# Kernel tuning notes

Measured on AMD Instinct MI355X. Metric: run time of the kernel, lower is better.

## Reference

```python
import jax, jax.numpy as jnp
import numpy as np

B, CIR_LEN, AUX_DIM, T, CD, DS, DCONV = 16, 16384, 14, 512, 256, 16, 4
SEG = CIR_LEN // T          # 32
DI = 2 * CD                 # d_inner = 512


def layer_norm(x, g, b, eps=1e-5):
    m = jnp.mean(x, -1, keepdims=True)
    v = jnp.var(x, -1, keepdims=True)
    return (x - m) * jax.lax.rsqrt(v + eps) * g + b


def gelu(x):
    return jax.nn.gelu(x, approximate=False)  # torch default exact GELU


def selective_ssm(x, in_proj_w, conv_w, conv_b, x_proj_w, dt_proj_w, dt_proj_b, A_log, D, out_proj_w):
    # x: (B, L, CD)
    Bsz, L, _ = x.shape
    xz = x @ in_proj_w.T                      # (B, L, 2*DI)
    x_in, z = jnp.split(xz, 2, axis=-1)       # each (B, L, DI)
    # depthwise causal conv (pad d_conv-1 left, truncate to L == torch pad both + [:L])
    xp = jnp.pad(x_in, ((0, 0), (DCONV - 1, 0), (0, 0)))
    x_conv = sum(xp[:, k:k + L, :] * conv_w[:, k] for k in range(DCONV)) + conv_b
    x_conv = jax.nn.silu(x_conv)              # (B, L, DI)
    ssm_in = x_conv @ x_proj_w.T              # (B, L, 1+2*DS)
    dt_raw = ssm_in[..., :1]
    B_ssm = ssm_in[..., 1:1 + DS]             # (B, L, DS)
    C_ssm = ssm_in[..., 1 + DS:]              # (B, L, DS)
    delta = jax.nn.softplus(dt_raw @ dt_proj_w.T + dt_proj_b)      # (B, L, DI)
    A = -jnp.exp(A_log)                                            # (DI, DS)
    deltaA = jnp.exp(delta[..., None] * A)                         # (B, L, DI, DS)
    deltaB_u = delta[..., None] * B_ssm[:, :, None, :] * x_conv[..., None]

    def step(h, inp):
        dA, dBu, c = inp
        h = dA * h + dBu                       # (B, DI, DS)
        y = jnp.einsum('bds,bs->bd', h, c)     # (B, DI)
        return h, y

    h0 = jnp.zeros((Bsz, DI, DS), x.dtype)
    _, ys = jax.lax.scan(step, h0, (jnp.moveaxis(deltaA, 1, 0),
                                    jnp.moveaxis(deltaB_u, 1, 0),
                                    jnp.moveaxis(C_ssm, 1, 0)))
    y = jnp.moveaxis(ys, 0, 1)                 # (B, L, DI)
    y = y + x_conv * D
    y = y * jax.nn.silu(z)
    return y @ out_proj_w.T                    # (B, L, CD)


def setup_inputs() -> dict:
    key = jax.random.key(0)
    ks = iter(jax.random.split(key, 32))
    rn = lambda shape, s=0.02: jax.random.normal(next(ks), shape, jnp.float32) * s
    return {
        'cir': jax.random.normal(next(ks), (B, CIR_LEN), jnp.float32),
        'aux': jax.random.normal(next(ks), (B, AUX_DIM), jnp.float32),
        'cir_proj_w': rn((CD, SEG)),
        'cir_norm_g': jnp.ones((CD,)), 'cir_norm_b': jnp.zeros((CD,)),
        'aux_proj_w': rn((CD, AUX_DIM)),
        'aux_norm_g': jnp.ones((CD,)), 'aux_norm_b': jnp.zeros((CD,)),
        'm_norm_g': jnp.ones((CD,)), 'm_norm_b': jnp.zeros((CD,)),
        'in_proj_w': rn((2 * DI, CD)),
        'conv_w': rn((DI, DCONV)), 'conv_b': jnp.zeros((DI,)),
        'x_proj_w': rn((1 + 2 * DS, DI)),
        'dt_proj_w': rn((DI, 1)), 'dt_proj_b': jnp.zeros((DI,)),
        'A_log': jnp.log(jnp.broadcast_to(jnp.arange(1, DS + 1, dtype=jnp.float32), (DI, DS))),
        'D': jnp.ones((DI,)),
        'out_proj_w': rn((CD, DI)),
        'mid_w': rn((CD, CD)), 'mid_b': jnp.zeros((CD,)),
        'mid_norm_g': jnp.ones((CD,)), 'mid_norm_b': jnp.zeros((CD,)),
        'bn_g': jnp.ones((CD,)), 'bn_b': jnp.zeros((CD,)),
        'fc1_w': rn((CD // 2, CD)), 'fc1_b': jnp.zeros((CD // 2,)),
        'fc2_w': rn((1, CD // 2)), 'fc2_b': jnp.zeros((1,)),
    }


def reference(cir, aux, cir_proj_w, cir_norm_g, cir_norm_b, aux_proj_w, aux_norm_g, aux_norm_b,
              m_norm_g, m_norm_b, in_proj_w, conv_w, conv_b, x_proj_w, dt_proj_w, dt_proj_b,
              A_log, D, out_proj_w, mid_w, mid_b, mid_norm_g, mid_norm_b, bn_g, bn_b,
              fc1_w, fc1_b, fc2_w, fc2_b):
    # eval mode: dropout = identity, BatchNorm uses running stats (mean 0, var 1)
    x_seg = cir.reshape(cir.shape[0], T, SEG)
    h_cir = gelu(layer_norm(x_seg @ cir_proj_w.T, cir_norm_g, cir_norm_b))
    h_aux = gelu(layer_norm(aux @ aux_proj_w.T, aux_norm_g, aux_norm_b))[:, None, :]
    h = h_cir + h_aux                          # (B, T, CD)
    h = h + selective_ssm(layer_norm(h, m_norm_g, m_norm_b), in_proj_w, conv_w, conv_b,
                          x_proj_w, dt_proj_w, dt_proj_b, A_log, D, out_proj_w)
    hp = jnp.mean(h, axis=1)                   # AdaptiveAvgPool1d(1)
    h2 = gelu(layer_norm(hp @ mid_w.T + mid_b, mid_norm_g, mid_norm_b))
    hbn = h2 * jax.lax.rsqrt(jnp.float32(1.0 + 1e-5)) * bn_g + bn_b
    h3 = gelu(hbn @ fc1_w.T + fc1_b)
    return (h3 @ fc2_w.T + fc2_b)[:, 0]
```

## Files before the change

kernel.cpp:

```cpp
#include <hip/hip_runtime.h>
#include <hip/hip_bf16.h>

typedef __hip_bfloat16 bf16;
typedef __attribute__((ext_vector_type(8))) short short8;
typedef __attribute__((ext_vector_type(4))) float f32x4;

#define Bsz   16
#define Tn    512
#define SEG   32
#define CD    256
#define DI    512
#define DS    16
#define DCONV 4
#define BT    (Bsz*Tn)
#define NPART 32

__device__ __forceinline__ float erf_fast(float x) {
  float ax = fabsf(x);
  float t = 1.0f / (1.0f + 0.3275911f * ax);
  float p = t * (0.254829592f + t * (-0.284496736f + t * (1.421413741f +
            t * (-1.453152027f + t * 1.061405429f))));
  float r = 1.0f - p * __expf(-ax * ax);
  return copysignf(r, x);
}
__device__ __forceinline__ float gelu_f(float x) {
  return 0.5f * x * (1.0f + erf_fast(x * 0.7071067811865476f));
}
__device__ __forceinline__ float silu_f(float x) {
  return x / (1.0f + __expf(-x));
}
__device__ __forceinline__ float softplus_f(float x) {
  return fmaxf(x, 0.0f) + __logf(1.0f + __expf(-fabsf(x)));
}
__device__ __forceinline__ float bfu(unsigned short u) {
  return __uint_as_float(((unsigned int)u) << 16);
}
__device__ __forceinline__ unsigned short f2bfu(float x) {
  bf16 h = __float2bfloat16(x);
  return *(unsigned short*)&h;
}
__device__ __forceinline__ float block_sum256(float v, float* red) {
  int tid = threadIdx.x;
  #pragma unroll
  for (int off = 32; off > 0; off >>= 1) v += __shfl_down(v, off, 64);
  __syncthreads();
  if ((tid & 63) == 0) red[tid >> 6] = v;
  __syncthreads();
  return red[0] + red[1] + red[2] + red[3];
}

__global__ __launch_bounds__(256) void prep_kernel(
    const float* __restrict__ aux, const float* __restrict__ apw,
    const float* __restrict__ g, const float* __restrict__ bb,
    const float* __restrict__ in_w, const float* __restrict__ xpw,
    const float* __restrict__ cpw,
    bf16* __restrict__ w_in, bf16* __restrict__ wpad, bf16* __restrict__ cpwT,
    float* __restrict__ haux)
{
  __shared__ float red[4];
  int i = blockIdx.x * 256 + threadIdx.x;
  if (i < 262144) {
    int e = i & 7, lane = (i >> 3) & 63, k0 = (i >> 9) & 7, nb = i >> 12;
    int fr = lane & 15, q = lane >> 4;
    w_in[i] = __float2bfloat16(in_w[(size_t)(nb * 16 + fr) * 256 + k0 * 32 + q * 8 + e]);
  } else if (i < 294912) {
    int o = i - 262144;
    int e = o & 7, lane = (o >> 3) & 63, k0 = (o >> 9) & 15, nb = o >> 13;
    int fr = lane & 15, q = lane >> 4;
    int row = nb * 16 + fr, k = k0 * 32 + q * 8 + e;
    float v = 0.f;
    if (row < 32)       v = xpw[(1 + row) * 512 + k];
    else if (row == 32) v = xpw[k];
    wpad[o] = __float2bfloat16(v);
  } else {
    int o = i - 294912;
    int k = o >> 8, j = o & 255;
    cpwT[o] = __float2bfloat16(cpw[j * 32 + k]);
  }
  if (blockIdx.x < 16) {
    int b = blockIdx.x, j = threadIdx.x;
    float acc = 0.f;
    #pragma unroll
    for (int k = 0; k < 14; ++k)
      acc += aux[b * 14 + k] * apw[j * 14 + k];
    float s1 = block_sum256(acc, red);
    float s2 = block_sum256(acc * acc, red);
    float mean = s1 * (1.f / 256.f);
    float var  = s2 * (1.f / 256.f) - mean * mean;
    float xn = (acc - mean) * rsqrtf(var + 1e-5f) * g[j] + bb[j];
    haux[b * 256 + j] = gelu_f(xn);
  }
}

__global__ __launch_bounds__(512) void row_inproj_kernel(
    const float* __restrict__ cir, const bf16* __restrict__ cpwT,
    const float* __restrict__ cg, const float* __restrict__ cb,
    const float* __restrict__ mg, const float* __restrict__ mb,
    const float* __restrict__ haux, const bf16* __restrict__ w_in,
    bf16* __restrict__ xzbf, float* __restrict__ hp_part)
{
  __shared__ float hps[8][256];
  __shared__ __align__(16) unsigned short xns[16][264];
  int tid = threadIdx.x;
  int wave = tid >> 6, lane = tid & 63;
  int r0 = blockIdx.x * 16 + wave * 2;
  int b = blockIdx.x >> 5;
  int j0 = lane * 4;

  float vj[2][4] = {};
  for (int c = 0; c < 8; ++c) {
    float xk[2][4];
    #pragma unroll
    for (int r4 = 0; r4 < 2; ++r4) {
      float4 xv = ((const float4*)(cir + (size_t)(r0 + r4) * SEG))[c];
      xk[r4][0] = xv.x; xk[r4][1] = xv.y; xk[r4][2] = xv.z; xk[r4][3] = xv.w;
    }
    #pragma unroll
    for (int kk = 0; kk < 4; ++kk) {
      int k = c * 4 + kk;
      uint2 wv = *(const uint2*)((const unsigned short*)cpwT + k * 256 + j0);
      float w0 = __uint_as_float(wv.x << 16);
      float w1 = __uint_as_float(wv.x & 0xffff0000u);
      float w2 = __uint_as_float(wv.y << 16);
      float w3 = __uint_as_float(wv.y & 0xffff0000u);
      #pragma unroll
      for (int r4 = 0; r4 < 2; ++r4) {
        float xv = xk[r4][kk];
        vj[r4][0] += xv * w0; vj[r4][1] += xv * w1;
        vj[r4][2] += xv * w2; vj[r4][3] += xv * w3;
      }
    }
  }
  float s[2], q2[2];
  #pragma unroll
  for (int r4 = 0; r4 < 2; ++r4) {
    s[r4]  = vj[r4][0] + vj[r4][1] + vj[r4][2] + vj[r4][3];
    q2[r4] = vj[r4][0]*vj[r4][0] + vj[r4][1]*vj[r4][1]
           + vj[r4][2]*vj[r4][2] + vj[r4][3]*vj[r4][3];
  }
  #pragma unroll
  for (int off = 32; off > 0; off >>= 1) {
    #pragma unroll
    for (int r4 = 0; r4 < 2; ++r4) {
      s[r4]  += __shfl_xor(s[r4],  off, 64);
      q2[r4] += __shfl_xor(q2[r4], off, 64);
    }
  }
  float4 cgv = *(const float4*)(cg + j0);
  float4 cbv = *(const float4*)(cb + j0);
  float4 hxv = *(const float4*)(haux + b * 256 + j0);
  float hv[2][4];
  float hs[2], hq[2];
  #pragma unroll
  for (int r4 = 0; r4 < 2; ++r4) {
    float mean = s[r4] * (1.f/256.f);
    float var  = q2[r4] * (1.f/256.f) - mean * mean;
    float inv  = rsqrtf(var + 1e-5f);
    float g0 = gelu_f((vj[r4][0] - mean) * inv * cgv.x + cbv.x) + hxv.x;
    float g1 = gelu_f((vj[r4][1] - mean) * inv * cgv.y + cbv.y) + hxv.y;
    float g2 = gelu_f((vj[r4][2] - mean) * inv * cgv.z + cbv.z) + hxv.z;
    float g3 = gelu_f((vj[r4][3] - mean) * inv * cgv.w + cbv.w) + hxv.w;
    hv[r4][0] = g0; hv[r4][1] = g1; hv[r4][2] = g2; hv[r4][3] = g3;
    hs[r4] = g0 + g1 + g2 + g3;
    hq[r4] = g0*g0 + g1*g1 + g2*g2 + g3*g3;
  }
  #pragma unroll
  for (int off = 32; off > 0; off >>= 1) {
    #pragma unroll
    for (int r4 = 0; r4 < 2; ++r4) {
      hs[r4] += __shfl_xor(hs[r4], off, 64);
      hq[r4] += __shfl_xor(hq[r4], off, 64);
    }
  }
  float4 mgv = *(const float4*)(mg + j0);
  float4 mbv = *(const float4*)(mb + j0);
  #pragma unroll
  for (int r4 = 0; r4 < 2; ++r4) {
    float m2  = hs[r4] * (1.f/256.f);
    float v2  = hq[r4] * (1.f/256.f) - m2 * m2;
    float inv2 = rsqrtf(v2 + 1e-5f);
    unsigned int lo = (unsigned int)f2bfu((hv[r4][0] - m2) * inv2 * mgv.x + mbv.x) |
                      ((unsigned int)f2bfu((hv[r4][1] - m2) * inv2 * mgv.y + mbv.y) << 16);
    unsigned int hi = (unsigned int)f2bfu((hv[r4][2] - m2) * inv2 * mgv.z + mbv.z) |
                      ((unsigned int)f2bfu((hv[r4][3] - m2) * inv2 * mgv.w + mbv.w) << 16);
    uint2 pk; pk.x = lo; pk.y = hi;
    *(uint2*)&xns[wave * 2 + r4][j0] = pk;
  }
  #pragma unroll
  for (int q = 0; q < 4; ++q)
    hps[wave][j0 + q] = hv[0][q] + hv[1][q];
  __syncthreads();
  if (tid < 256) {
    int j = tid;
    float part = hps[0][j] + hps[1][j] + hps[2][j] + hps[3][j]
               + hps[4][j] + hps[5][j] + hps[6][j] + hps[7][j];
    hp_part[(size_t)(blockIdx.x & (NPART - 1)) * 4096 + b * 256 + j] =
        part * (1.f / 512.f);
  }
  {
    int fr = lane & 15, quad = lane >> 4;
    int rbase = blockIdx.x * 16;
    const short* Wp = (const short*)w_in;
    unsigned short* xzp = (unsigned short*)xzbf;
    #pragma unroll
    for (int nt = 0; nt < 8; ++nt) {
      int nb = wave * 8 + nt;
      f32x4 acc = {0.f, 0.f, 0.f, 0.f};
      #pragma unroll
      for (int k0 = 0; k0 < 8; ++k0) {
        int ka = k0 * 32 + quad * 8;
        short8 a = *(const short8*)&xns[fr][ka];
        short8 bb8 = *(const short8*)(Wp + (((size_t)nb * 8 + k0) * 64 + lane) * 8);
        acc = __builtin_amdgcn_mfma_f32_16x16x32_bf16(a, bb8, acc, 0, 0, 0);
      }
      int n0 = nb * 16;
      int crow = quad * 4;
      #pragma unroll
      for (int i = 0; i < 4; ++i)
        xzp[(size_t)(rbase + crow + i) * 1024 + n0 + fr] = f2bfu(acc[i]);
    }
  }
}

__global__ __launch_bounds__(512) void conv_xproj_kernel(
    const bf16* __restrict__ xzbf, const bf16* __restrict__ wpad,
    const float* __restrict__ cw, const float* __restrict__ cbv,
    float* __restrict__ ssm)
{
  __shared__ __align__(16) unsigned short xst[35][512];
  __shared__ __align__(16) unsigned short xcs[32][520];
  int c = blockIdx.x, b = blockIdx.y;
  int t0 = c * 32;
  int tid = threadIdx.x;
  const unsigned short* xzp = (const unsigned short*)xzbf;

  for (int it = tid; it < 2240; it += 512) {
    int row = it >> 6, c8 = it & 63;
    int t = t0 - 3 + row;
    uint4 v = make_uint4(0u, 0u, 0u, 0u);
    if (t >= 0)
      v = *(const uint4*)(xzp + ((size_t)((b << 9) + t)) * 1024 + c8 * 8);
    *(uint4*)&xst[row][c8 * 8] = v;
  }
  __syncthreads();

  {
    int d = tid;
    float4 w = *(const float4*)(cw + d * 4);
    float cbd = cbv[d];
    float pa = bfu(xst[0][d]), pb = bfu(xst[1][d]), pc = bfu(xst[2][d]);
    #pragma unroll
    for (int i = 0; i < 32; ++i) {
      float x = bfu(xst[3 + i][d]);
      float a = cbd + w.x * pa + w.y * pb + w.z * pc + w.w * x;
      pa = pb; pb = pc; pc = x;
      xcs[i][d] = f2bfu(silu_f(a));
    }
  }
  __syncthreads();

  {
    int wave = tid >> 6, lane = tid & 63;
    int fr = lane & 15, quad = lane >> 4;
    int mh = wave >> 2;
    int nb = wave & 3;
    int n0 = nb * 16;
    f32x4 acc = {0.f, 0.f, 0.f, 0.f};
    const short* Wp = (const short*)wpad;
    #pragma unroll
    for (int k0 = 0; k0 < 16; ++k0) {
      int ka = k0 * 32 + quad * 8;
      short8 a = *(const short8*)&xcs[mh * 16 + fr][ka];
      short8 b8 = *(const short8*)(Wp + (((size_t)nb * 16 + k0) * 64 + lane) * 8);
      acc = __builtin_amdgcn_mfma_f32_16x16x32_bf16(a, b8, acc, 0, 0, 0);
    }
    int ccol = lane & 15, crow = quad * 4;
    #pragma unroll
    for (int i = 0; i < 4; ++i)
      ssm[((size_t)((b << 9) + t0 + mh * 16 + crow + i)) * 64 + n0 + ccol] = acc[i];
  }
}

__global__ __launch_bounds__(512) void scan_full_kernel(
    const bf16* __restrict__ xzbf, const float* __restrict__ ssm,
    const float* __restrict__ cw, const float* __restrict__ cbv,
    const float* __restrict__ dtw, const float* __restrict__ dtb,
    const float* __restrict__ A_log, const float* __restrict__ Dd,
    float* __restrict__ ybar)
{
  __shared__ __align__(16) unsigned short xraw[67][32];
  __shared__ __align__(8)  float BC[64][34];
  __shared__ float dts[64];
  __shared__ __align__(16) float cgd[64][32][4];
  __shared__ float xdp_s[16][32];

  int dgrp = blockIdx.x, b = blockIdx.y;
  int tid = threadIdx.x;
  int d0 = dgrp * 32;
  int bb = b << 9;
  const unsigned short* xzp = (const unsigned short*)xzbf;

  int s  = tid & 15;
  int dp = tid >> 4;
  int dS = d0 + dp;
  float As  = -__expf(A_log[dS * 16 + s]);
  int d2 = tid & 31, r16 = tid >> 5;
  int dC = d0 + d2;
  float4 wc = *(const float4*)(cw + dC * 4);
  float cbd = cbv[dC];
  float wdC = dtw[dC], bdC = dtb[dC];

  float h = 0.f, yacc = 0.f, xdp = 0.f;

  for (int tile = 0; tile < 8; ++tile) {
    int t0 = tile * 64;
    __syncthreads();
    if (tid < 268) {
      int row = tid >> 2, c4 = tid & 3;
      int t = t0 - 3 + row;
      uint4 v = make_uint4(0u, 0u, 0u, 0u);
      if (t >= 0)
        v = *(const uint4*)(xzp + ((size_t)(bb + t)) * 1024 + d0 + c4 * 8);
      *(uint4*)&xraw[row][c4 * 8] = v;
    }
    {
      int r = tid >> 3, l8 = tid & 7;
      const float* srow = ssm + ((size_t)(bb + t0 + r)) * 64;
      float4 v = *(const float4*)(srow + l8 * 4);
      int cc = l8 * 4;
      if (cc < 16) {
        BC[r][cc*2]   = v.x; BC[r][cc*2+2] = v.y;
        BC[r][cc*2+4] = v.z; BC[r][cc*2+6] = v.w;
      } else {
        int c2 = cc - 16;
        BC[r][c2*2+1] = v.x; BC[r][c2*2+3] = v.y;
        BC[r][c2*2+5] = v.z; BC[r][c2*2+7] = v.w;
      }
      if (l8 == 0) dts[r] = srow[32];
    }
    float zr[4];
    #pragma unroll
    for (int jj = 0; jj < 4; ++jj) {
      int ii = jj * 16 + r16;
      zr[jj] = bfu(xzp[((size_t)(bb + t0 + ii)) * 1024 + 512 + dC]);
    }
    __syncthreads();
    #pragma unroll
    for (int jj = 0; jj < 4; ++jj) {
      int ii = jj * 16 + r16;
      float xa = bfu(xraw[ii][d2]);
      float xb = bfu(xraw[ii + 1][d2]);
      float xm = bfu(xraw[ii + 2][d2]);
      float xd = bfu(xraw[ii + 3][d2]);
      float a = cbd + wc.x * xa + wc.y * xb + wc.z * xm + wc.w * xd;
      float xc = bfu(f2bfu(silu_f(a)));
      float gt = silu_f(zr[jj]);
      float de = softplus_f(dts[ii] * wdC + bdC);
      xdp += xc * gt;
      float4 pk; pk.x = de * xc; pk.y = gt; pk.z = de; pk.w = 0.f;
      *(float4*)&cgd[ii][d2][0] = pk;
    }
    __syncthreads();
    #pragma unroll 8
    for (int i = 0; i < 64; ++i) {
      float4 cg = *(const float4*)&cgd[i][dp][0];
      float2 bc = *(const float2*)&BC[i][s * 2];
      float a = __expf(As * cg.z);
      h = a * h + cg.x * bc.x;
      yacc += h * (bc.y * cg.y);
    }
  }
  xdp_s[r16][d2] = xdp;
  yacc += __shfl_xor(yacc, 1, 64);
  yacc += __shfl_xor(yacc, 2, 64);
  yacc += __shfl_xor(yacc, 4, 64);
  yacc += __shfl_xor(yacc, 8, 64);
  __syncthreads();
  if (s == 0) {
    float xds = 0.f;
    #pragma unroll
    for (int k = 0; k < 16; ++k) xds += xdp_s[k][dp];
    ybar[b * 512 + dS] = yacc + Dd[dS] * xds;
  }
}

__global__ __launch_bounds__(256) void head_kernel(
    const float* __restrict__ hp_part, const float* __restrict__ ybar,
    const float* __restrict__ w_out,
    const float* __restrict__ midw, const float* __restrict__ midb,
    const float* __restrict__ mng, const float* __restrict__ mnb,
    const float* __restrict__ bng, const float* __restrict__ bnb,
    const float* __restrict__ f1w, const float* __restrict__ f1b,
    const float* __restrict__ f2w, const float* __restrict__ f2b,
    float* __restrict__ out)
{
  __shared__ float red[4];
  __shared__ __align__(16) float yb[512];
  __shared__ __align__(16) float shp[256];
  __shared__ __align__(16) float sh[256];
  __shared__ __align__(16) float sh2[128];
  int b = blockIdx.x, j = threadIdx.x;
  yb[j]       = ybar[b * 512 + j];
  yb[256 + j] = ybar[b * 512 + 256 + j];
  float hv = 0.f;
  #pragma unroll
  for (int p = 0; p < NPART; ++p)
    hv += hp_part[(size_t)p * 4096 + b * 256 + j];
  __syncthreads();
  {
    float acc2 = 0.f;
    const float4* wr = (const float4*)(w_out + j * 512);
    const float4* yv = (const float4*)yb;
    #pragma unroll 4
    for (int k = 0; k < 128; ++k) {
      float4 w = wr[k], x = yv[k];
      acc2 += w.x * x.x + w.y * x.y + w.z * x.z + w.w * x.w;
    }
    hv += acc2 * (1.f / 512.f);
  }
  shp[j] = hv;
  __syncthreads();
  float acc = midb[j];
  {
    const float4* mw = (const float4*)(midw + j * 256);
    const float4* sv = (const float4*)shp;
    #pragma unroll 4
    for (int k = 0; k < 64; ++k) {
      float4 w = mw[k], xv = sv[k];
      acc += w.x * xv.x + w.y * xv.y + w.z * xv.z + w.w * xv.w;
    }
  }
  float s1 = block_sum256(acc, red);
  float s2 = block_sum256(acc * acc, red);
  float mean = s1 * (1.f / 256.f);
  float var  = s2 * (1.f / 256.f) - mean * mean;
  float h2 = gelu_f((acc - mean) * rsqrtf(var + 1e-5f) * mng[j] + mnb[j]);
  float hbn = h2 * rsqrtf(1.0f + 1e-5f) * bng[j] + bnb[j];
  sh[j] = hbn;
  __syncthreads();
  if (j < 128) {
    float a2 = f1b[j];
    const float4* fw = (const float4*)(f1w + j * 256);
    const float4* sv = (const float4*)sh;
    #pragma unroll 4
    for (int k = 0; k < 64; ++k) {
      float4 w = fw[k], xv = sv[k];
      a2 += w.x * xv.x + w.y * xv.y + w.z * xv.z + w.w * xv.w;
    }
    sh2[j] = gelu_f(a2);
  }
  __syncthreads();
  if (j == 0) {
    float o = f2b[0];
    const float4* fw = (const float4*)f2w;
    const float4* sv = (const float4*)sh2;
    for (int k = 0; k < 32; ++k) {
      float4 w = fw[k], xv = sv[k];
      o += w.x * xv.x + w.y * xv.y + w.z * xv.z + w.w * xv.w;
    }
    out[b] = o;
  }
}

extern "C" void kernel_launch(void* const* d_in, const int* in_sizes, int n_in,
                              void* d_out, int out_size, void* d_ws, size_t ws_size,
                              hipStream_t stream)
{
  const float* cir        = (const float*)d_in[0];
  const float* aux        = (const float*)d_in[1];
  const float* cir_proj_w = (const float*)d_in[2];
  const float* cir_norm_g = (const float*)d_in[3];
  const float* cir_norm_b = (const float*)d_in[4];
  const float* aux_proj_w = (const float*)d_in[5];
  const float* aux_norm_g = (const float*)d_in[6];
  const float* aux_norm_b = (const float*)d_in[7];
  const float* m_norm_g   = (const float*)d_in[8];
  const float* m_norm_b   = (const float*)d_in[9];
  const float* in_proj_w  = (const float*)d_in[10];
  const float* conv_w     = (const float*)d_in[11];
  const float* conv_b     = (const float*)d_in[12];
  const float* x_proj_w   = (const float*)d_in[13];
  const float* dt_proj_w  = (const float*)d_in[14];
  const float* dt_proj_b  = (const float*)d_in[15];
  const float* A_log      = (const float*)d_in[16];
  const float* Dd         = (const float*)d_in[17];
  const float* out_proj_w = (const float*)d_in[18];
  const float* mid_w      = (const float*)d_in[19];
  const float* mid_b      = (const float*)d_in[20];
  const float* mid_norm_g = (const float*)d_in[21];
  const float* mid_norm_b = (const float*)d_in[22];
  const float* bn_g       = (const float*)d_in[23];
  const float* bn_b       = (const float*)d_in[24];
  const float* fc1_w      = (const float*)d_in[25];
  const float* fc1_b      = (const float*)d_in[26];
  const float* fc2_w      = (const float*)d_in[27];
  const float* fc2_b      = (const float*)d_in[28];
  float* out = (float*)d_out;

  float* ws      = (float*)d_ws;
  bf16*  xzbf    = (bf16*)ws;
  float* ssm     = ws + 4194304;
  bf16*  w_inbf  = (bf16*)(ssm + 524288);
  bf16*  wpadbf  = (bf16*)((float*)w_inbf + 131072);
  bf16*  cpwTbf  = (bf16*)((float*)wpadbf + 16384);
  float* haux    = (float*)cpwTbf + 4096;
  float* hp_part = haux + 4096;
  float* ybar    = hp_part + 131072;

  prep_kernel<<<1184, 256, 0, stream>>>(aux, aux_proj_w, aux_norm_g, aux_norm_b,
                                        in_proj_w, x_proj_w, cir_proj_w,
                                        w_inbf, wpadbf, cpwTbf, haux);
  row_inproj_kernel<<<512, 512, 0, stream>>>(cir, cpwTbf, cir_norm_g, cir_norm_b,
                                             m_norm_g, m_norm_b, haux, w_inbf,
                                             xzbf, hp_part);
  conv_xproj_kernel<<<dim3(16, Bsz), 512, 0, stream>>>(xzbf, wpadbf, conv_w, conv_b,
                                                       ssm);
  scan_full_kernel<<<dim3(16, Bsz), 512, 0, stream>>>(xzbf, ssm, conv_w, conv_b,
                                                      dt_proj_w, dt_proj_b,
                                                      A_log, Dd, ybar);
  head_kernel<<<16, 256, 0, stream>>>(hp_part, ybar, out_proj_w,
                                      mid_w, mid_b, mid_norm_g, mid_norm_b,
                                      bn_g, bn_b, fc1_w, fc1_b, fc2_w, fc2_b, out);
}
```

Before: 223.4 us.

## Split SSM scan into two time halves combined via carried decay products

The sequential scan over 512 timesteps is split into two halves of 256 processed concurrently by two groups of 512 threads in a 1024-thread block. The second half starts from zero state and accumulates a running decay product P and a weighted sum K, so the first half's final state can be folded in afterward as hendA*K. This halves the serial dependency chain per thread and doubles thread-level parallelism on the latency-bound scan. The cost is extra multiply work in the second half, twice the shared memory for double-width tiles, and higher register pressure under the 1024-thread launch bound.

```diff
diff --git a/kernel.cpp b/kernel.cpp
--- a/kernel.cpp
+++ b/kernel.cpp
@@ -281,18 +281,21 @@
   }
 }
 
-__global__ __launch_bounds__(512) void scan_full_kernel(
+__global__ __launch_bounds__(1024) void scan_full_kernel(
     const bf16* __restrict__ xzbf, const float* __restrict__ ssm,
     const float* __restrict__ cw, const float* __restrict__ cbv,
     const float* __restrict__ dtw, const float* __restrict__ dtb,
     const float* __restrict__ A_log, const float* __restrict__ Dd,
     float* __restrict__ ybar)
 {
-  __shared__ __align__(16) unsigned short xraw[67][32];
-  __shared__ __align__(8)  float BC[64][34];
-  __shared__ float dts[64];
-  __shared__ __align__(16) float cgd[64][32][4];
-  __shared__ float xdp_s[16][32];
+  __shared__ __align__(16) unsigned short xraw[2][35][32];
+  __shared__ __align__(16) unsigned short zraw[2][32][32];
+  __shared__ __align__(8)  float BC[2][32][34];
+  __shared__ float dts[2][32];
+  __shared__ __align__(16) float cgd[2][32][32][4];
+  __shared__ float xdp_s[32][32];
+  __shared__ float hendA[32][16];
+  __shared__ float ybh[2][32];
 
   int dgrp = blockIdx.x, b = blockIdx.y;
   int tid = threadIdx.x;
@@ -301,86 +304,100 @@
   const unsigned short* xzp = (const unsigned short*)xzbf;
 
   int s  = tid & 15;
-  int dp = tid >> 4;
+  int dp = (tid >> 4) & 31;
+  int qh = tid >> 9;
   int dS = d0 + dp;
   float As  = -__expf(A_log[dS * 16 + s]);
-  int d2 = tid & 31, r16 = tid >> 5;
+  int d2 = tid & 31, r32 = (tid >> 5) & 31;
   int dC = d0 + d2;
   float4 wc = *(const float4*)(cw + dC * 4);
   float cbd = cbv[dC];
   float wdC = dtw[dC], bdC = dtb[dC];
 
-  float h = 0.f, yacc = 0.f, xdp = 0.f;
-
-  for (int tile = 0; tile < 8; ++tile) {
-    int t0 = tile * 64;
+  float h = 0.f, yacc = 0.f, P = 1.f, K = 0.f, xdp = 0.f;
+
+  for (int p = 0; p < 8; ++p) {
     __syncthreads();
-    if (tid < 268) {
-      int row = tid >> 2, c4 = tid & 3;
-      int t = t0 - 3 + row;
-      uint4 v = make_uint4(0u, 0u, 0u, 0u);
-      if (t >= 0)
-        v = *(const uint4*)(xzp + ((size_t)(bb + t)) * 1024 + d0 + c4 * 8);
-      *(uint4*)&xraw[row][c4 * 8] = v;
-    }
-    {
-      int r = tid >> 3, l8 = tid & 7;
-      const float* srow = ssm + ((size_t)(bb + t0 + r)) * 64;
+    if (tid < 512) {
+      for (int it = tid; it < 536; it += 512) {
+        int q = it >= 268;
+        int e = it - (q ? 268 : 0);
+        int t0q = q * 256 + p * 32;
+        if (e < 140) {
+          int row = e >> 2, c4 = e & 3;
+          int t = t0q - 3 + row;
+          uint4 v = make_uint4(0u, 0u, 0u, 0u);
+          if (t >= 0)
+            v = *(const uint4*)(xzp + (size_t)(bb + t) * 1024 + d0 + c4 * 8);
+          *(uint4*)&xraw[q][row][c4 * 8] = v;
+        } else {
+          int e2 = e - 140;
+          int row = e2 >> 2, c4 = e2 & 3;
+          uint4 v = *(const uint4*)(xzp + (size_t)(bb + t0q + row) * 1024 + 512 + d0 + c4 * 8);
+          *(uint4*)&zraw[q][row][c4 * 8] = v;
+        }
+      }
+    } else {
+      int t2 = tid - 512;
+      int q = t2 >> 8;
+      int r = (t2 >> 3) & 31, l8 = t2 & 7;
+      int t0q = q * 256 + p * 32;
+      const float* srow = ssm + (size_t)(bb + t0q + r) * 64;
       float4 v = *(const float4*)(srow + l8 * 4);
       int cc = l8 * 4;
       if (cc < 16) {
-        BC[r][cc*2]   = v.x; BC[r][cc*2+2] = v.y;
-        BC[r][cc*2+4] = v.z; BC[r][cc*2+6] = v.w;
+        BC[q][r][cc*2]   = v.x; BC[q][r][cc*2+2] = v.y;
+        BC[q][r][cc*2+4] = v.z; BC[q][r][cc*2+6] = v.w;
       } else {
         int c2 = cc - 16;
-        BC[r][c2*2+1] = v.x; BC[r][c2*2+3] = v.y;
-        BC[r][c2*2+5] = v.z; BC[r][c2*2+7] = v.w;
+        BC[q][r][c2*2+1] = v.x; BC[q][r][c2*2+3] = v.y;
+        BC[q][r][c2*2+5] = v.z; BC[q][r][c2*2+7] = v.w;
       }
-      if (l8 == 0) dts[r] = srow[32];
-    }
-    float zr[4];
-    #pragma unroll
-    for (int jj = 0; jj < 4; ++jj) {
-      int ii = jj * 16 + r16;
-      zr[jj] = bfu(xzp[((size_t)(bb + t0 + ii)) * 1024 + 512 + dC]);
+      if (l8 == 0) dts[q][r] = srow[32];
     }
     __syncthreads();
     #pragma unroll
-    for (int jj = 0; jj < 4; ++jj) {
-      int ii = jj * 16 + r16;
-      float xa = bfu(xraw[ii][d2]);
-      float xb = bfu(xraw[ii + 1][d2]);
-      float xm = bfu(xraw[ii + 2][d2]);
-      float xd = bfu(xraw[ii + 3][d2]);
+    for (int q = 0; q < 2; ++q) {
+      int ii = r32;
+      float xa = bfu(xraw[q][ii][d2]);
+      float xb = bfu(xraw[q][ii + 1][d2]);
+      float xm = bfu(xraw[q][ii + 2][d2]);
+      float xd = bfu(xraw[q][ii + 3][d2]);
       float a = cbd + wc.x * xa + wc.y * xb + wc.z * xm + wc.w * xd;
       float xc = bfu(f2bfu(silu_f(a)));
-      float gt = silu_f(zr[jj]);
-      float de = softplus_f(dts[ii] * wdC + bdC);
+      float gt = silu_f(bfu(zraw[q][ii][d2]));
+      float de = softplus_f(dts[q][ii] * wdC + bdC);
       xdp += xc * gt;
       float4 pk; pk.x = de * xc; pk.y = gt; pk.z = de; pk.w = 0.f;
-      *(float4*)&cgd[ii][d2][0] = pk;
+      *(float4*)&cgd[q][ii][d2][0] = pk;
     }
     __syncthreads();
-    #pragma unroll 8
-    for (int i = 0; i < 64; ++i) {
-      float4 cg = *(const float4*)&cgd[i][dp][0];
-      float2 bc = *(const float2*)&BC[i][s * 2];
+    #pragma unroll
+    for (int i = 0; i < 32; ++i) {
+      float4 cg = *(const float4*)&cgd[qh][i][dp][0];
+      float2 bc = *(const float2*)&BC[qh][i][s * 2];
       float a = __expf(As * cg.z);
       h = a * h + cg.x * bc.x;
-      yacc += h * (bc.y * cg.y);
-    }
-  }
-  xdp_s[r16][d2] = xdp;
+      float w = bc.y * cg.y;
+      yacc += h * w;
+      if (qh) { P *= a; K += P * w; }
+    }
+  }
+  xdp_s[r32][d2] = xdp;
+  if (qh == 0) hendA[dp][s] = h;
+  __syncthreads();
+  if (qh == 1) yacc += hendA[dp][s] * K;
   yacc += __shfl_xor(yacc, 1, 64);
   yacc += __shfl_xor(yacc, 2, 64);
   yacc += __shfl_xor(yacc, 4, 64);
   yacc += __shfl_xor(yacc, 8, 64);
-  __syncthreads();
-  if (s == 0) {
+  if (s == 0) ybh[qh][dp] = yacc;
+  __syncthreads();
+  if (qh == 0 && s == 0) {
     float xds = 0.f;
     #pragma unroll
-    for (int k = 0; k < 16; ++k) xds += xdp_s[k][dp];
-    ybar[b * 512 + dS] = yacc + Dd[dS] * xds;
+    for (int k = 0; k < 32; ++k) xds += xdp_s[k][dp];
+    ybar[b * 512 + dS] = ybh[0][dp] + ybh[1][dp] + Dd[dS] * xds;
   }
 }
 
@@ -515,9 +532,9 @@
                                              xzbf, hp_part);
   conv_xproj_kernel<<<dim3(16, Bsz), 512, 0, stream>>>(xzbf, wpadbf, conv_w, conv_b,
                                                        ssm);
-  scan_full_kernel<<<dim3(16, Bsz), 512, 0, stream>>>(xzbf, ssm, conv_w, conv_b,
-                                                      dt_proj_w, dt_proj_b,
-                                                      A_log, Dd, ybar);
+  scan_full_kernel<<<dim3(16, Bsz), 1024, 0, stream>>>(xzbf, ssm, conv_w, conv_b,
+                                                       dt_proj_w, dt_proj_b,
+                                                       A_log, Dd, ybar);
   head_kernel<<<16, 256, 0, stream>>>(hp_part, ybar, out_proj_w,
                                       mid_w, mid_b, mid_norm_g, mid_norm_b,
                                       bn_g, bn_b, fc1_w, fc1_b, fc2_w, fc2_b, out);
```

Measured after the change: 215.0 us. -3.7%, faster.
